# Kernel optimization log

Measured on AMD Instinct MI355X. Metric: run time of the kernel, lower is better.

## Reference

```python
import jax, jax.numpy as jnp
import numpy as np

B, N, M, C = 1024, 2048, 128, 512
EPS = 1e-8


def setup_inputs() -> dict:
    key = jax.random.key(0)
    k1, k2, k3, k4, k5 = jax.random.split(key, 5)
    x = jax.random.normal(k1, (B, C), dtype=jnp.float32)
    u = jax.random.uniform(k2, (B, N), dtype=jnp.float32) + 1e-3
    w_prev = u / jnp.sum(u, axis=1, keepdims=True)  # valid attention distribution
    mem = jax.random.normal(k3, (B, N, M), dtype=jnp.float32)
    # xavier-uniform-ish fc_read weight (gain 1.4), tiny-std bias
    limit = 1.4 * np.sqrt(6.0 / (C + (M + 6)))
    W = jax.random.uniform(k4, (M + 6, C), dtype=jnp.float32, minval=-limit, maxval=limit)
    b = 0.01 * jax.random.normal(k5, (M + 6,), dtype=jnp.float32)
    return {"x": x, "w_prev": w_prev, "mem": mem, "W": W, "b": b}


def reference(x, w_prev, mem, W, b):
    m = mem.shape[-1]
    o = x @ W.T + b                                   # [B, M+6]
    k = o[:, :m]                                      # key [B, M]
    beta = jax.nn.softplus(o[:, m:m + 1])             # [B, 1]
    g = jax.nn.sigmoid(o[:, m + 1:m + 2])             # [B, 1]
    s = jax.nn.softmax(o[:, m + 2:m + 5], axis=1)     # [B, 3] shift weights
    gamma = 1.0 + jax.nn.softplus(o[:, m + 5:m + 6])  # [B, 1]

    # content addressing: cosine similarity, beta-sharpened softmax
    dot = jnp.einsum('bnm,bm->bn', mem, k)
    denom = jnp.linalg.norm(mem, axis=-1) * jnp.linalg.norm(k, axis=-1, keepdims=True) + EPS
    w_c = jax.nn.softmax(beta * (dot / denom), axis=1)  # [B, N]

    # gate interpolation
    w_g = g * w_c + (1.0 - g) * w_prev

    # circular convolution with 3-tap shift: w_t[i] = sum_j s[j] * w_g[(i+j-1) mod N]
    w_t = (s[:, 0:1] * jnp.roll(w_g, 1, axis=1)
           + s[:, 1:2] * w_g
           + s[:, 2:3] * jnp.roll(w_g, -1, axis=1))

    # sharpening
    w_pow = w_t ** gamma
    w = w_pow / (jnp.sum(w_pow, axis=1, keepdims=True) + 1e-16)

    # weighted read
    r = jnp.einsum('bn,bnm->bm', w, mem)
    return (r, w)
```

## Files before the change

### kernel.cpp

```cpp
#include <hip/hip_runtime.h>
#include <math.h>

#define B 1024
#define N 2048
#define M 128
#define C 512
#define OD (M + 6)
#define EPSF 1e-8f
#define CHUNK 256
#define NCHUNK 8
#define NGRP 64
#define ITERS (B / NGRP)
#define GRID_F (NCHUNK * NGRP)
#define AGENT __HIP_MEMORY_SCOPE_AGENT

__device__ __forceinline__ float softplusf(float x) {
    return fmaxf(x, 0.f) + log1pf(expf(-fabsf(x)));
}
__device__ __forceinline__ float sigmoidf_(float x) {
    return 1.f / (1.f + expf(-x));
}

__device__ __forceinline__ void bar_lds() {
    asm volatile("s_waitcnt lgkmcnt(0)" ::: "memory");
    __builtin_amdgcn_s_barrier();
}

__global__ __launch_bounds__(256) void k_head(
    const float* __restrict__ x, const float* __restrict__ W,
    const float* __restrict__ bias, float* __restrict__ kbuf,
    float* __restrict__ params)
{
    const int b = blockIdx.x;
    __shared__ float xs[C];
    __shared__ float os[OD];
    __shared__ float red[128];

    for (int i = threadIdx.x; i < C; i += 256) xs[i] = x[(size_t)b * C + i];
    __syncthreads();

    if (threadIdx.x < OD) {
        const int j = threadIdx.x;
        const float4* wr = (const float4*)(W + (size_t)j * C);
        float acc = 0.f;
#pragma unroll 8
        for (int c = 0; c < C / 4; ++c) {
            float4 wv = wr[c];
            acc = fmaf(wv.x, xs[4 * c + 0], acc);
            acc = fmaf(wv.y, xs[4 * c + 1], acc);
            acc = fmaf(wv.z, xs[4 * c + 2], acc);
            acc = fmaf(wv.w, xs[4 * c + 3], acc);
        }
        os[j] = acc + bias[j];
    }
    __syncthreads();

    if (threadIdx.x < M) {
        float v = os[threadIdx.x];
        kbuf[(size_t)b * M + threadIdx.x] = v;
        red[threadIdx.x] = v * v;
    }
    __syncthreads();
    for (int s = 64; s > 0; s >>= 1) {
        if (threadIdx.x < s) red[threadIdx.x] += red[threadIdx.x + s];
        __syncthreads();
    }
    if (threadIdx.x == 0) {
        float kn = sqrtf(red[0]);
        float beta = softplusf(os[M]);
        float g = sigmoidf_(os[M + 1]);
        float a0 = os[M + 2], a1 = os[M + 3], a2 = os[M + 4];
        float mx = fmaxf(a0, fmaxf(a1, a2));
        float e0 = expf(a0 - mx), e1 = expf(a1 - mx), e2 = expf(a2 - mx);
        float inv = 1.f / (e0 + e1 + e2);
        float gamma = 1.f + softplusf(os[M + 5]);
        float* p = params + (size_t)b * 8;
        p[0] = beta; p[1] = g; p[2] = e0 * inv; p[3] = e1 * inv;
        p[4] = e2 * inv; p[5] = gamma; p[6] = kn; p[7] = 0.f;
    }
}

__global__ __launch_bounds__(1024, 8) void k_fused(
    const float* __restrict__ mem, const float* __restrict__ kbuf,
    const float* __restrict__ params, const float* __restrict__ w_prev,
    float* __restrict__ w_out,
    float* __restrict__ sPart, float* __restrict__ tPart,
    int* __restrict__ cnt1, float* __restrict__ edgeE,
    float* __restrict__ rpart)
{
    __shared__ float2 redT[CHUNK * 17];
    __shared__ float eA[CHUNK];
    __shared__ float wgA[CHUNK + 2];
    __shared__ float pwA[CHUNK];
    __shared__ float redA[16 * 128];
    __shared__ float partS[4];
    __shared__ float partT[4];
    __shared__ float bcast[4];

    const int tid  = threadIdx.x;
    const int lane = tid & 63;
    const int wv   = tid >> 6;
    const int half = lane >> 5;
    const int l32  = lane & 31;
    const int hw   = wv * 2 + half;

    const int cid  = blockIdx.x >> 6;
    const int bgrp = blockIdx.x & 63;

    for (int it = 0; it < ITERS; ++it) {
        const int b = bgrp * ITERS + it;
        const float* cb = mem + ((size_t)b * N + cid * CHUNK) * M;

        float4 frag[8];
#pragma unroll
        for (int j = 0; j < 8; ++j)
            frag[j] = ((const float4*)(cb + (size_t)(hw * 8 + j) * M))[l32];

        float wp_t = 0.f, wpL = 0.f, wpR = 0.f;
        if (tid < CHUNK)
            wp_t = w_prev[(size_t)b * N + cid * CHUNK + tid];
        if (tid == 0) {
            wpL = w_prev[(size_t)b * N + ((cid * CHUNK + N - 1) & (N - 1))];
            wpR = w_prev[(size_t)b * N + ((cid * CHUNK + CHUNK) & (N - 1))];
        }
        const float4 kv = ((const float4*)(kbuf + (size_t)b * M))[l32];
        const float4 p0 = ((const float4*)(params + (size_t)b * 8))[0];
        const float4 p1 = ((const float4*)(params + (size_t)b * 8))[1];
        const float beta = p0.x, kn = p1.z;

#pragma unroll
        for (int j = 0; j < 8; ++j) {
            const float4 f = frag[j];
            float dt = f.x * kv.x + f.y * kv.y + f.z * kv.z + f.w * kv.w;
            float sq = f.x * f.x + f.y * f.y + f.z * f.z + f.w * f.w;
            dt += __shfl_xor(dt, 16, 64);
            sq += __shfl_xor(sq, 16, 64);
            if (l32 < 16)
                redT[(hw * 8 + j) * 17 + l32] = make_float2(dt, sq);
        }
        bar_lds();

        {
            float e = 0.f;
            if (tid < CHUNK) {
                const float2* rowp = &redT[tid * 17];
                float dt = 0.f, sq = 0.f;
#pragma unroll
                for (int g2 = 0; g2 < 16; ++g2) { dt += rowp[g2].x; sq += rowp[g2].y; }
                const float z = beta * dt / (sqrtf(sq) * kn + EPSF);
                e = expf(z);
                eA[tid] = e;
            }
            float myS = e;
#pragma unroll
            for (int s = 32; s >= 1; s >>= 1) myS += __shfl_xor(myS, s, 64);
            if (lane == 0 && wv < 4) partS[wv] = myS;
        }
        bar_lds();

        if (tid == 0) {
            const float S = partS[0] + partS[1] + partS[2] + partS[3];
            __hip_atomic_store(&sPart[(size_t)b * NCHUNK + cid], S, __ATOMIC_RELAXED, AGENT);
            __hip_atomic_store(&edgeE[((size_t)b * NCHUNK + cid) * 2 + 0], eA[0], __ATOMIC_RELAXED, AGENT);
            __hip_atomic_store(&edgeE[((size_t)b * NCHUNK + cid) * 2 + 1], eA[CHUNK - 1], __ATOMIC_RELAXED, AGENT);
            asm volatile("s_waitcnt vmcnt(0)" ::: "memory");
            __hip_atomic_fetch_add(&cnt1[b], 1, __ATOMIC_RELAXED, AGENT);
            int tries = 0;
            while (__hip_atomic_load(&cnt1[b], __ATOMIC_RELAXED, AGENT) < NCHUNK) {
                __builtin_amdgcn_s_sleep(1);
                if (++tries > (1 << 22)) break;
            }
            float St = 0.f;
#pragma unroll
            for (int c2 = 0; c2 < NCHUNK; ++c2)
                St += __hip_atomic_load(&sPart[(size_t)b * NCHUNK + c2], __ATOMIC_RELAXED, AGENT);
            bcast[0] = 1.f / St;
            bcast[1] = __hip_atomic_load(&edgeE[((size_t)b * NCHUNK + ((cid + NCHUNK - 1) & (NCHUNK - 1))) * 2 + 1], __ATOMIC_RELAXED, AGENT);
            bcast[2] = __hip_atomic_load(&edgeE[((size_t)b * NCHUNK + ((cid + 1) & (NCHUNK - 1))) * 2 + 0], __ATOMIC_RELAXED, AGENT);
        }
        bar_lds();

        const float invS = bcast[0], eL = bcast[1], eR = bcast[2];
        const float g = p0.y, s0p = p0.z, s1p = p0.w, s2p = p1.x, gamma = p1.y;
        if (tid < CHUNK)
            wgA[tid + 1] = g * eA[tid] * invS + (1.f - g) * wp_t;
        if (tid == 0) {
            wgA[0]         = g * eL * invS + (1.f - g) * wpL;
            wgA[CHUNK + 1] = g * eR * invS + (1.f - g) * wpR;
        }
        bar_lds();

        float myT = 0.f;
        if (tid < CHUNK) {
            const float wt = s0p * wgA[tid] + s1p * wgA[tid + 1] + s2p * wgA[tid + 2];
            const float pw = powf(wt, gamma);
            pwA[tid] = pw;
            myT = pw;
        }
#pragma unroll
        for (int s = 32; s >= 1; s >>= 1) myT += __shfl_xor(myT, s, 64);
        if (lane == 0 && wv < 4) partT[wv] = myT;
        bar_lds();

        if (tid == 0)
            tPart[(size_t)b * NCHUNK + cid] = partT[0] + partT[1] + partT[2] + partT[3];

        {
            float4 pwv[2];
#pragma unroll
            for (int q4 = 0; q4 < 2; ++q4)
                pwv[q4] = ((const float4*)&pwA[hw * 8])[q4];
            float4 acc = make_float4(0.f, 0.f, 0.f, 0.f);
#pragma unroll
            for (int j = 0; j < 8; ++j) {
                const float pw = ((const float*)&pwv[j >> 2])[j & 3];
                acc.x = fmaf(pw, frag[j].x, acc.x);
                acc.y = fmaf(pw, frag[j].y, acc.y);
                acc.z = fmaf(pw, frag[j].z, acc.z);
                acc.w = fmaf(pw, frag[j].w, acc.w);
            }
            acc.x += __shfl_xor(acc.x, 32, 64);
            acc.y += __shfl_xor(acc.y, 32, 64);
            acc.z += __shfl_xor(acc.z, 32, 64);
            acc.w += __shfl_xor(acc.w, 32, 64);
            if (half == 0) *(float4*)&redA[wv * 128 + l32 * 4] = acc;
        }
        bar_lds();

        if (tid < 128) {
            float s = 0.f;
#pragma unroll
            for (int w2 = 0; w2 < 16; ++w2) s += redA[w2 * 128 + tid];
            rpart[((size_t)b * NCHUNK + cid) * 128 + tid] = s;
        }
        if (tid < CHUNK)
            w_out[(size_t)b * N + cid * CHUNK + tid] = pwA[tid];
        bar_lds();
    }
}

__global__ __launch_bounds__(256) void k_norm(
    const float* __restrict__ tPart, const float* __restrict__ rpart,
    float* __restrict__ w_out, float* __restrict__ r_out)
{
    const int b = blockIdx.x, tid = threadIdx.x;
    float T = 0.f;
#pragma unroll
    for (int c = 0; c < NCHUNK; ++c) T += tPart[(size_t)b * NCHUNK + c];
    const float invT = 1.f / (T + 1e-16f);

    float4* w4 = (float4*)(w_out + (size_t)b * N);
#pragma unroll
    for (int k = 0; k < 2; ++k) {
        float4 v = w4[tid + k * 256];
        v.x *= invT; v.y *= invT; v.z *= invT; v.w *= invT;
        w4[tid + k * 256] = v;
    }
    if (tid < 128) {
        float s = 0.f;
#pragma unroll
        for (int c = 0; c < NCHUNK; ++c)
            s += rpart[((size_t)b * NCHUNK + c) * 128 + tid];
        r_out[(size_t)b * M + tid] = s * invT;
    }
}

extern "C" void kernel_launch(void* const* d_in, const int* in_sizes, int n_in,
                              void* d_out, int out_size, void* d_ws, size_t ws_size,
                              hipStream_t stream) {
    const float* x      = (const float*)d_in[0];
    const float* w_prev = (const float*)d_in[1];
    const float* mem    = (const float*)d_in[2];
    const float* W      = (const float*)d_in[3];
    const float* bias   = (const float*)d_in[4];

    float* r_out = (float*)d_out;
    float* w_out = (float*)d_out + (size_t)B * M;

    float* ws     = (float*)d_ws;
    float* kbuf   = ws;
    float* params = kbuf + (size_t)B * M;
    float* sPart  = params + (size_t)B * 8;
    float* tPart  = sPart + (size_t)B * NCHUNK;
    int*   cnt1   = (int*)(tPart + (size_t)B * NCHUNK);
    float* edgeE  = (float*)(cnt1 + B);
    float* rpart  = edgeE + (size_t)B * NCHUNK * 2;

    hipMemsetAsync(cnt1, 0, B * sizeof(int), stream);

    k_head<<<B, 256, 0, stream>>>(x, W, bias, kbuf, params);
    k_fused<<<GRID_F, 1024, 0, stream>>>(mem, kbuf, params, w_prev, w_out,
                                         sPart, tPart, cnt1, edgeE, rpart);
    k_norm<<<B, 256, 0, stream>>>(tPart, rpart, w_out, r_out);
}
```

Measured before the change: 348.6 us.

## Double-buffer memory rows across two wave groups to prefetch next batch

Splits each 1024-thread block into two 8-wave groups that take turns: one group computes on the current batch row's memory chunk while the other prefetches the next batch's chunk into registers. The grid shrinks to 256 blocks, each with 32 iterations, and every wave now holds 16 rows instead of 8. The goal is to hide global-load latency behind the softmax, cross-block sync and reduction work. It also switches exp and pow to the fast intrinsics and drops the trailing barrier, which raises register pressure and lowers occupancy, and may introduce LDS hazards or precision differences.

```diff
diff --git a/kernel.cpp b/kernel.cpp
--- a/kernel.cpp
+++ b/kernel.cpp
@@ -9,9 +9,9 @@
 #define EPSF 1e-8f
 #define CHUNK 256
 #define NCHUNK 8
-#define NGRP 64
-#define ITERS (B / NGRP)
-#define GRID_F (NCHUNK * NGRP)
+#define NGRP 32
+#define ITERS 32
+#define GRID_F 256
 #define AGENT __HIP_MEMORY_SCOPE_AGENT
 
 __device__ __forceinline__ float softplusf(float x) {
@@ -80,7 +80,7 @@
     }
 }
 
-__global__ __launch_bounds__(1024, 8) void k_fused(
+__global__ __launch_bounds__(1024, 4) void k_fused(
     const float* __restrict__ mem, const float* __restrict__ kbuf,
     const float* __restrict__ params, const float* __restrict__ w_prev,
     float* __restrict__ w_out,
@@ -92,29 +92,48 @@
     __shared__ float eA[CHUNK];
     __shared__ float wgA[CHUNK + 2];
     __shared__ float pwA[CHUNK];
-    __shared__ float redA[16 * 128];
-    __shared__ float partS[4];
+    __shared__ float redA[8 * 128];
+    __shared__ float partS[8];
     __shared__ float partT[4];
     __shared__ float bcast[4];
 
     const int tid  = threadIdx.x;
     const int lane = tid & 63;
     const int wv   = tid >> 6;
+    const int grp  = wv >> 3;
+    const int lwv  = wv & 7;
     const int half = lane >> 5;
     const int l32  = lane & 31;
-    const int hw   = wv * 2 + half;
-
-    const int cid  = blockIdx.x >> 6;
-    const int bgrp = blockIdx.x & 63;
+    const int lhw  = lwv * 2 + half;
+
+    const int cid  = blockIdx.x >> 5;
+    const int bgrp = blockIdx.x & 31;
+
+    float4 frag[16];
+    float4 kv = make_float4(0.f, 0.f, 0.f, 0.f);
+
+    if (grp == 0) {
+        const int b0 = bgrp * ITERS;
+        const float* cb = mem + ((size_t)b0 * N + cid * CHUNK) * M;
+#pragma unroll
+        for (int j = 0; j < 16; ++j)
+            frag[j] = ((const float4*)(cb + (size_t)(lhw * 16 + j) * M))[l32];
+        kv = ((const float4*)(kbuf + (size_t)b0 * M))[l32];
+    }
 
     for (int it = 0; it < ITERS; ++it) {
         const int b = bgrp * ITERS + it;
-        const float* cb = mem + ((size_t)b * N + cid * CHUNK) * M;
-
-        float4 frag[8];
-#pragma unroll
-        for (int j = 0; j < 8; ++j)
-            frag[j] = ((const float4*)(cb + (size_t)(hw * 8 + j) * M))[l32];
+        const bool own = (grp == (it & 1));
+        const int pubw = (it & 1) ? 8 : 0;
+
+        if (!own) {
+            const int bn = (it + 1 < ITERS) ? (b + 1) : b;
+            const float* nb = mem + ((size_t)bn * N + cid * CHUNK) * M;
+#pragma unroll
+            for (int j = 0; j < 16; ++j)
+                frag[j] = ((const float4*)(nb + (size_t)(lhw * 16 + j) * M))[l32];
+            kv = ((const float4*)(kbuf + (size_t)bn * M))[l32];
+        }
 
         float wp_t = 0.f, wpL = 0.f, wpR = 0.f;
         if (tid < CHUNK)
@@ -123,43 +142,51 @@
             wpL = w_prev[(size_t)b * N + ((cid * CHUNK + N - 1) & (N - 1))];
             wpR = w_prev[(size_t)b * N + ((cid * CHUNK + CHUNK) & (N - 1))];
         }
-        const float4 kv = ((const float4*)(kbuf + (size_t)b * M))[l32];
         const float4 p0 = ((const float4*)(params + (size_t)b * 8))[0];
         const float4 p1 = ((const float4*)(params + (size_t)b * 8))[1];
         const float beta = p0.x, kn = p1.z;
 
-#pragma unroll
-        for (int j = 0; j < 8; ++j) {
-            const float4 f = frag[j];
-            float dt = f.x * kv.x + f.y * kv.y + f.z * kv.z + f.w * kv.w;
-            float sq = f.x * f.x + f.y * f.y + f.z * f.z + f.w * f.w;
-            dt += __shfl_xor(dt, 16, 64);
-            sq += __shfl_xor(sq, 16, 64);
-            if (l32 < 16)
-                redT[(hw * 8 + j) * 17 + l32] = make_float2(dt, sq);
+        if (own) {
+#pragma unroll
+            for (int j = 0; j < 16; ++j) {
+                const float4 f = frag[j];
+                float dt = f.x * kv.x + f.y * kv.y + f.z * kv.z + f.w * kv.w;
+                float sq = f.x * f.x + f.y * f.y + f.z * f.z + f.w * f.w;
+                dt += __shfl_xor(dt, 16, 64);
+                sq += __shfl_xor(sq, 16, 64);
+                if (l32 < 16)
+                    redT[(lhw * 16 + j) * 17 + l32] = make_float2(dt, sq);
+            }
         }
         bar_lds();
 
         {
             float e = 0.f;
-            if (tid < CHUNK) {
-                const float2* rowp = &redT[tid * 17];
+            if (tid < 2 * CHUNK) {
+                const int r = tid >> 1, q = tid & 1;
+                const float2* rowp = &redT[r * 17 + q * 8];
                 float dt = 0.f, sq = 0.f;
 #pragma unroll
-                for (int g2 = 0; g2 < 16; ++g2) { dt += rowp[g2].x; sq += rowp[g2].y; }
-                const float z = beta * dt / (sqrtf(sq) * kn + EPSF);
-                e = expf(z);
-                eA[tid] = e;
+                for (int g2 = 0; g2 < 8; ++g2) { dt += rowp[g2].x; sq += rowp[g2].y; }
+                dt += __shfl_xor(dt, 1, 64);
+                sq += __shfl_xor(sq, 1, 64);
+                if (q == 0) {
+                    const float z = beta * dt / (sqrtf(sq) * kn + EPSF);
+                    e = __expf(z);
+                    eA[r] = e;
+                }
             }
             float myS = e;
 #pragma unroll
             for (int s = 32; s >= 1; s >>= 1) myS += __shfl_xor(myS, s, 64);
-            if (lane == 0 && wv < 4) partS[wv] = myS;
-        }
-        bar_lds();
-
-        if (tid == 0) {
-            const float S = partS[0] + partS[1] + partS[2] + partS[3];
+            if (lane == 0 && wv < 8) partS[wv] = myS;
+        }
+        bar_lds();
+
+        if (lane == 0 && wv == pubw) {
+            float S = 0.f;
+#pragma unroll
+            for (int h = 0; h < 8; ++h) S += partS[h];
             __hip_atomic_store(&sPart[(size_t)b * NCHUNK + cid], S, __ATOMIC_RELAXED, AGENT);
             __hip_atomic_store(&edgeE[((size_t)b * NCHUNK + cid) * 2 + 0], eA[0], __ATOMIC_RELAXED, AGENT);
             __hip_atomic_store(&edgeE[((size_t)b * NCHUNK + cid) * 2 + 1], eA[CHUNK - 1], __ATOMIC_RELAXED, AGENT);
@@ -193,7 +220,7 @@
         float myT = 0.f;
         if (tid < CHUNK) {
             const float wt = s0p * wgA[tid] + s1p * wgA[tid + 1] + s2p * wgA[tid + 2];
-            const float pw = powf(wt, gamma);
+            const float pw = __powf(wt, gamma);
             pwA[tid] = pw;
             myT = pw;
         }
@@ -205,14 +232,14 @@
         if (tid == 0)
             tPart[(size_t)b * NCHUNK + cid] = partT[0] + partT[1] + partT[2] + partT[3];
 
-        {
-            float4 pwv[2];
-#pragma unroll
-            for (int q4 = 0; q4 < 2; ++q4)
-                pwv[q4] = ((const float4*)&pwA[hw * 8])[q4];
+        if (own) {
+            float4 pwv[4];
+#pragma unroll
+            for (int q4 = 0; q4 < 4; ++q4)
+                pwv[q4] = ((const float4*)&pwA[lhw * 16])[q4];
             float4 acc = make_float4(0.f, 0.f, 0.f, 0.f);
 #pragma unroll
-            for (int j = 0; j < 8; ++j) {
+            for (int j = 0; j < 16; ++j) {
                 const float pw = ((const float*)&pwv[j >> 2])[j & 3];
                 acc.x = fmaf(pw, frag[j].x, acc.x);
                 acc.y = fmaf(pw, frag[j].y, acc.y);
@@ -223,19 +250,18 @@
             acc.y += __shfl_xor(acc.y, 32, 64);
             acc.z += __shfl_xor(acc.z, 32, 64);
             acc.w += __shfl_xor(acc.w, 32, 64);
-            if (half == 0) *(float4*)&redA[wv * 128 + l32 * 4] = acc;
+            if (half == 0) *(float4*)&redA[lwv * 128 + l32 * 4] = acc;
         }
         bar_lds();
 
         if (tid < 128) {
             float s = 0.f;
 #pragma unroll
-            for (int w2 = 0; w2 < 16; ++w2) s += redA[w2 * 128 + tid];
+            for (int w2 = 0; w2 < 8; ++w2) s += redA[w2 * 128 + tid];
             rpart[((size_t)b * NCHUNK + cid) * 128 + tid] = s;
         }
         if (tid < CHUNK)
             w_out[(size_t)b * N + cid * CHUNK + tid] = pwA[tid];
-        bar_lds();
     }
 }
 
```

Measured after the change: 328.9 us. 5.6% less time.

## Prefetch next batch's memory chunk into LDS via async global-to-LDS loads

Applied to the files above, without the earlier changes.

Each block now copies its whole 256x128 memory chunk (128 KB) into shared memory with global_load_lds and starts the copy for the next batch while the current batch runs its cross-block softmax sync and sharpening. Frag values are read back from LDS instead of from global memory. The grid is halved to 256 blocks doing 32 iterations each, and the dot/norm reduction gains an extra shuffle step so it needs fewer LDS partials. Fast-math __expf and __powf replace expf and powf, which lowers accuracy slightly. The large LDS footprint limits occupancy to one block per CU and halves total parallelism, so the gain depends on hiding load latency.

```diff
diff --git a/kernel.cpp b/kernel.cpp
--- a/kernel.cpp
+++ b/kernel.cpp
@@ -9,10 +9,12 @@
 #define EPSF 1e-8f
 #define CHUNK 256
 #define NCHUNK 8
-#define NGRP 64
-#define ITERS (B / NGRP)
-#define GRID_F (NCHUNK * NGRP)
+#define NGRP 32
+#define ITERS 32
+#define GRID_F 256
 #define AGENT __HIP_MEMORY_SCOPE_AGENT
+
+typedef unsigned int u32;
 
 __device__ __forceinline__ float softplusf(float x) {
     return fmaxf(x, 0.f) + log1pf(expf(-fabsf(x)));
@@ -21,8 +23,18 @@
     return 1.f / (1.f + expf(-x));
 }
 
+__device__ __forceinline__ void g2lds16(const float* gsrc, float* ldst) {
+    __builtin_amdgcn_global_load_lds(
+        (const __attribute__((address_space(1))) u32*)gsrc,
+        (__attribute__((address_space(3))) u32*)ldst, 16, 0, 0);
+}
+
 __device__ __forceinline__ void bar_lds() {
     asm volatile("s_waitcnt lgkmcnt(0)" ::: "memory");
+    __builtin_amdgcn_s_barrier();
+}
+__device__ __forceinline__ void bar_full() {
+    asm volatile("s_waitcnt vmcnt(0) lgkmcnt(0)" ::: "memory");
     __builtin_amdgcn_s_barrier();
 }
 
@@ -80,7 +92,7 @@
     }
 }
 
-__global__ __launch_bounds__(1024, 8) void k_fused(
+__global__ __launch_bounds__(1024, 4) void k_fused(
     const float* __restrict__ mem, const float* __restrict__ kbuf,
     const float* __restrict__ params, const float* __restrict__ w_prev,
     float* __restrict__ w_out,
@@ -88,14 +100,15 @@
     int* __restrict__ cnt1, float* __restrict__ edgeE,
     float* __restrict__ rpart)
 {
-    __shared__ float2 redT[CHUNK * 17];
+    __shared__ float stage[CHUNK * M];
+    __shared__ float2 redT[CHUNK * 9];
     __shared__ float eA[CHUNK];
     __shared__ float wgA[CHUNK + 2];
     __shared__ float pwA[CHUNK];
-    __shared__ float redA[16 * 128];
     __shared__ float partS[4];
     __shared__ float partT[4];
     __shared__ float bcast[4];
+    float* redA = (float*)redT;
 
     const int tid  = threadIdx.x;
     const int lane = tid & 63;
@@ -104,17 +117,22 @@
     const int l32  = lane & 31;
     const int hw   = wv * 2 + half;
 
-    const int cid  = blockIdx.x >> 6;
-    const int bgrp = blockIdx.x & 63;
+    const int cid  = blockIdx.x >> 5;
+    const int bgrp = blockIdx.x & 31;
+
+    {
+        const int b0 = bgrp * ITERS;
+        const float* cb = mem + ((size_t)b0 * N + cid * CHUNK) * M;
+#pragma unroll
+        for (int k = 0; k < 8; ++k)
+            g2lds16(cb + wv * 2048 + k * 256 + lane * 4, stage + wv * 2048 + k * 256);
+    }
 
     for (int it = 0; it < ITERS; ++it) {
         const int b = bgrp * ITERS + it;
-        const float* cb = mem + ((size_t)b * N + cid * CHUNK) * M;
-
-        float4 frag[8];
-#pragma unroll
-        for (int j = 0; j < 8; ++j)
-            frag[j] = ((const float4*)(cb + (size_t)(hw * 8 + j) * M))[l32];
+        const bool havenext = (it + 1 < ITERS);
+
+        bar_full();
 
         float wp_t = 0.f, wpL = 0.f, wpR = 0.f;
         if (tid < CHUNK)
@@ -128,27 +146,30 @@
         const float4 p1 = ((const float4*)(params + (size_t)b * 8))[1];
         const float beta = p0.x, kn = p1.z;
 
+        float4 frag[8];
 #pragma unroll
         for (int j = 0; j < 8; ++j) {
-            const float4 f = frag[j];
-            float dt = f.x * kv.x + f.y * kv.y + f.z * kv.z + f.w * kv.w;
-            float sq = f.x * f.x + f.y * f.y + f.z * f.z + f.w * f.w;
+            frag[j] = *(const float4*)&stage[(hw * 8 + j) * M + l32 * 4];
+            float dt = frag[j].x * kv.x + frag[j].y * kv.y + frag[j].z * kv.z + frag[j].w * kv.w;
+            float sq = frag[j].x * frag[j].x + frag[j].y * frag[j].y + frag[j].z * frag[j].z + frag[j].w * frag[j].w;
             dt += __shfl_xor(dt, 16, 64);
             sq += __shfl_xor(sq, 16, 64);
-            if (l32 < 16)
-                redT[(hw * 8 + j) * 17 + l32] = make_float2(dt, sq);
+            dt += __shfl_xor(dt, 8, 64);
+            sq += __shfl_xor(sq, 8, 64);
+            if (l32 < 8)
+                redT[(hw * 8 + j) * 9 + l32] = make_float2(dt, sq);
         }
         bar_lds();
 
         {
             float e = 0.f;
             if (tid < CHUNK) {
-                const float2* rowp = &redT[tid * 17];
+                const float2* rowp = &redT[tid * 9];
                 float dt = 0.f, sq = 0.f;
 #pragma unroll
-                for (int g2 = 0; g2 < 16; ++g2) { dt += rowp[g2].x; sq += rowp[g2].y; }
+                for (int g2 = 0; g2 < 8; ++g2) { dt += rowp[g2].x; sq += rowp[g2].y; }
                 const float z = beta * dt / (sqrtf(sq) * kn + EPSF);
-                e = expf(z);
+                e = __expf(z);
                 eA[tid] = e;
             }
             float myS = e;
@@ -157,6 +178,14 @@
             if (lane == 0 && wv < 4) partS[wv] = myS;
         }
         bar_lds();
+
+        const int bn = havenext ? (b + 1) : b;
+        const float* nb = mem + ((size_t)bn * N + cid * CHUNK) * M;
+        if (havenext && wv != 0) {
+#pragma unroll
+            for (int k = 0; k < 8; ++k)
+                g2lds16(nb + wv * 2048 + k * 256 + lane * 4, stage + wv * 2048 + k * 256);
+        }
 
         if (tid == 0) {
             const float S = partS[0] + partS[1] + partS[2] + partS[3];
@@ -180,6 +209,12 @@
         }
         bar_lds();
 
+        if (havenext && wv == 0) {
+#pragma unroll
+            for (int k = 0; k < 8; ++k)
+                g2lds16(nb + k * 256 + lane * 4, stage + k * 256);
+        }
+
         const float invS = bcast[0], eL = bcast[1], eR = bcast[2];
         const float g = p0.y, s0p = p0.z, s1p = p0.w, s2p = p1.x, gamma = p1.y;
         if (tid < CHUNK)
@@ -193,7 +228,7 @@
         float myT = 0.f;
         if (tid < CHUNK) {
             const float wt = s0p * wgA[tid] + s1p * wgA[tid + 1] + s2p * wgA[tid + 2];
-            const float pw = powf(wt, gamma);
+            const float pw = __powf(wt, gamma);
             pwA[tid] = pw;
             myT = pw;
         }
@@ -235,7 +270,6 @@
         }
         if (tid < CHUNK)
             w_out[(size_t)b * N + cid * CHUNK + tid] = pwA[tid];
-        bar_lds();
     }
 }
 
```

Result: slower. 380.1 us (+9.0%).
